# Kernel tuning notes

Hardware: AMD Instinct MI355X
Metric: run time of the kernel (lower is better)

The kernel has to match this reference:

```python
import math
import jax, jax.numpy as jnp
import numpy as np

B, H, W, CP = 64, 512, 512, 400
HALF_X = W // 2          # int, matches width//2 in the original
HALF_Y = H / 2.0         # float, matches height/2 in the original
NPTS = CP // 2
PI = math.pi


def fix_radians(tt):
    # Faithful translation of: -relu(-(2pi - relu(-tt)), threshold=-2pi) + relu(tt)
    inner = -(2.0 * PI - jnp.maximum(-tt, 0.0))
    thr = jnp.where(inner > -2.0 * PI, inner, 0.0)  # keras relu with threshold=-2pi
    return -thr + jnp.maximum(tt, 0.0)


def half_contour(pred_norm):
    # pred_norm: [B, H, W] in [0, 1]
    pred1st = jnp.round(pred_norm[:, :, :HALF_X])          # [B, H, W/2]
    x1st = jnp.sum(pred1st, axis=2)                        # [B, H] column count per row
    xaux = jnp.clip(x1st, 0.0, 1.0)                        # relu(.., threshold=0, max_value=1)
    ythtop = HALF_Y - jnp.sum(xaux[:, :HALF_X], axis=1)    # [B]
    ythbottom = HALF_Y + jnp.sum(xaux[:, HALF_X:], axis=1) # [B]
    rows = jnp.arange(W, dtype=pred_norm.dtype)[None, :]   # [1, W] (H == W assumed by original)
    # relu(rows - top) + top == max(rows, top); then min with bottom
    y1st = jnp.minimum(jnp.maximum(rows, ythtop[:, None]), ythbottom[:, None])  # [B, W]
    # Original: x1st <- half_x - x1st, then cart2pol(x1st - half_x, y1st - half_y)
    xc = -x1st                                             # [B, H]
    yc = y1st - HALF_Y                                     # [B, W]
    r1st = jnp.sqrt(xc ** 2 + yc ** 2)                     # [B, H]
    tt1st = fix_radians(jnp.arctan2(yc, xc))               # [B, H]

    tt_new = (PI / 2.0) + jnp.arange(NPTS, dtype=pred_norm.dtype) * (PI / NPTS)  # [NPTS]

    # RBF angular smoothing (get_rbf_points), with periodic wraparound copies
    tt_1 = jnp.concatenate([tt1st - 2.0 * PI, tt1st, tt1st + 2.0 * PI], axis=1)  # [B, 3H]
    r_cat = jnp.concatenate([r1st, r1st, r1st], axis=1)                          # [B, 3H]
    d2 = (tt_1[:, :, None] - tt_new[None, None, :]) ** 2                         # [B, 3H, NPTS]
    d2 = jnp.minimum(d2, 1.0)
    wgt = jnp.exp(-100.0 * d2)                                                   # [B, 3H, NPTS]
    wgt = wgt / jnp.sum(wgt, axis=1, keepdims=True)
    r_new = jnp.einsum('bkn,bk->bn', wgt, r_cat)                                 # [B, NPTS]

    x_new = r_new * jnp.cos(tt_new)[None, :] + HALF_X
    y_new = r_new * jnp.sin(tt_new)[None, :] + HALF_Y
    return jnp.stack([x_new, y_new], axis=-1)              # [B, NPTS, 2]


def setup_inputs() -> dict:
    key = jax.random.key(0)
    inputs = jax.random.uniform(key, (B, H, W, 2), dtype=jnp.float32)
    return {"inputs": inputs}


def reference(inputs) -> jnp.ndarray:
    lvc = inputs[:, :, :, -1]                              # [B, H, W]
    mn = jnp.min(lvc, axis=(1, 2), keepdims=True)
    mx = jnp.max(lvc, axis=(1, 2), keepdims=True)
    lvc_norm = (lvc - mn) / (mx - mn)
    c1 = half_contour(lvc_norm)                            # [B, NPTS, 2]
    c2 = half_contour(lvc_norm[:, :, ::-1])                # mirrored half
    c2 = jnp.concatenate([float(H) - c2[:, :, :1], c2[:, :, 1:]], axis=-1)[:, ::-1, :]
    return jnp.concatenate([c1, c2], axis=1)               # [B, CP, 2]
```

## Files before the change

kernel.cpp:

```cpp
#include <hip/hip_runtime.h>
#include <math.h>
#include <float.h>

#define BB 64
#define HH 512
#define WW 512
#define NPTS 200

#define PMIN_OFF 0
#define PMAX_OFF 2048
#define CNT_OFF  4224
#define TT_OFF   69760
#define RR_OFF   135296
#define SUMR_OFF 200832

__global__ __launch_bounds__(256) void kminmax(const float* __restrict__ in,
                                               float* __restrict__ ws) {
    int bid = blockIdx.x;
    int b   = bid >> 5;
    int c   = bid & 31;
    int t   = threadIdx.x;
    const float4* base = (const float4*)in + (size_t)b * 131072 + (size_t)c * 4096;
    float vmin = FLT_MAX, vmax = -FLT_MAX;
#pragma unroll
    for (int i = 0; i < 16; ++i) {
        float4 v = base[i * 256 + t];
        vmin = fminf(vmin, fminf(v.y, v.w));
        vmax = fmaxf(vmax, fmaxf(v.y, v.w));
    }
    for (int m = 32; m >= 1; m >>= 1) {
        vmin = fminf(vmin, __shfl_xor(vmin, m, 64));
        vmax = fmaxf(vmax, __shfl_xor(vmax, m, 64));
    }
    __shared__ float smin[4], smax[4];
    int wv = t >> 6;
    if ((t & 63) == 0) { smin[wv] = vmin; smax[wv] = vmax; }
    __syncthreads();
    if (t == 0) {
        float a = fminf(fminf(smin[0], smin[1]), fminf(smin[2], smin[3]));
        float z = fmaxf(fmaxf(smax[0], smax[1]), fmaxf(smax[2], smax[3]));
        ws[PMIN_OFF + bid] = a;
        ws[PMAX_OFF + bid] = z;
    }
}

__global__ __launch_bounds__(256) void kcount(const float* __restrict__ in,
                                              float* __restrict__ ws) {
    int gwave = (blockIdx.x * 256 + threadIdx.x) >> 6;
    int lane  = threadIdx.x & 63;
    int b     = gwave >> 9;
    int row   = gwave & 511;

    float mn = ws[PMIN_OFF + b * 32 + (lane & 31)];
    float mx = ws[PMAX_OFF + b * 32 + (lane & 31)];
    for (int m = 16; m >= 1; m >>= 1) {
        mn = fminf(mn, __shfl_xor(mn, m, 64));
        mx = fmaxf(mx, __shfl_xor(mx, m, 64));
    }
    float den = mx - mn;

    const float4* base = (const float4*)in + ((size_t)(b * HH + row)) * 256;
    int cl = 0, cr = 0;
#pragma unroll
    for (int i = 0; i < 4; ++i) {
        float4 v = base[i * 64 + lane];
        float t0 = (v.y - mn) / den;
        float t1 = (v.w - mn) / den;
        int c = (int)rintf(t0) + (int)rintf(t1);
        if (i < 2) cl += c; else cr += c;
    }
    for (int m = 32; m >= 1; m >>= 1) {
        cl += __shfl_xor(cl, m, 64);
        cr += __shfl_xor(cr, m, 64);
    }
    if (lane == 0) {
        ws[CNT_OFF + (b * 2 + 0) * 512 + row] = (float)cl;
        ws[CNT_OFF + (b * 2 + 1) * 512 + row] = (float)cr;
    }
}

__global__ __launch_bounds__(256) void kpolar(float* __restrict__ ws) {
    const float TWO_PI_F = 6.28318530717958647692f;
    const float PI_F     = 3.14159265358979323846f;
    int b2 = blockIdx.x;
    int t  = threadIdx.x;
    const float* cnt = ws + CNT_OFF + b2 * 512;
    float* tt_out    = ws + TT_OFF  + b2 * 512;
    float* rr_out    = ws + RR_OFF  + b2 * 512;

    __shared__ float s_red[12];

    float c0 = cnt[t];
    float c1 = cnt[t + 256];

    int r0 = (c0 >= 1.0f) ? 1 : 0;
    int r1 = (c1 >= 1.0f) ? 1 : 0;
    for (int m = 32; m >= 1; m >>= 1) {
        r0 += __shfl_xor(r0, m, 64);
        r1 += __shfl_xor(r1, m, 64);
    }
    int wv = t >> 6;
    if ((t & 63) == 0) { s_red[wv] = (float)r0; s_red[4 + wv] = (float)r1; }
    __syncthreads();
    float ythtop    = 256.0f - (s_red[0] + s_red[1] + s_red[2] + s_red[3]);
    float ythbottom = 256.0f + (s_red[4] + s_red[5] + s_red[6] + s_red[7]);

    float sumr_local = 0.0f;
#pragma unroll
    for (int j = 0; j < 2; ++j) {
        int   r  = t + j * 256;
        float x1 = (j == 0) ? c0 : c1;
        float y1 = fminf(fmaxf((float)r, ythtop), ythbottom);
        float xc = -x1;
        float yc = y1 - 256.0f;
        float rr = sqrtf(xc * xc + yc * yc);
        float tt;
        if (x1 == 0.0f && yc == 0.0f) {
            tt = PI_F;
        } else {
            tt = atan2f(yc, xc);
            if (tt < 0.0f) tt += TWO_PI_F;
        }
        tt_out[r] = tt;
        rr_out[r] = rr;
        sumr_local += rr;
    }
    float sr = sumr_local;
    for (int m = 32; m >= 1; m >>= 1) sr += __shfl_xor(sr, m, 64);
    if ((t & 63) == 0) s_red[8 + wv] = sr;
    __syncthreads();
    if (t == 0)
        ws[SUMR_OFF + b2] = s_red[8] + s_red[9] + s_red[10] + s_red[11];
}

__global__ __launch_bounds__(256) void kpoints(const float* __restrict__ ws,
                                               float* __restrict__ out) {
    int w    = (blockIdx.x * 256 + threadIdx.x) >> 6;
    int lane = threadIdx.x & 63;
    int b2   = w / NPTS;
    int t    = w - b2 * NPTS;
    int b    = b2 >> 1;
    int half = b2 & 1;

    const float4* ttv = (const float4*)(ws + TT_OFF + b2 * 512);
    const float4* rrv = (const float4*)(ws + RR_OFF + b2 * 512);
    float4 ta = ttv[lane], tb = ttv[lane + 64];
    float4 ra = rrv[lane], rb = rrv[lane + 64];
    float tts[8] = {ta.x, ta.y, ta.z, ta.w, tb.x, tb.y, tb.z, tb.w};
    float rs[8]  = {ra.x, ra.y, ra.z, ra.w, rb.x, rb.y, rb.z, rb.w};

    float ttn = 1.5707963267948966f + (float)t * 0.015707963267948966f;

    float d2[8];
    float dmin = 1.0f;
#pragma unroll
    for (int i = 0; i < 8; ++i) {
        float d = tts[i] - ttn;
        d2[i] = fminf(d * d, 1.0f);
        dmin = fminf(dmin, d2[i]);
    }
    for (int m = 32; m >= 1; m >>= 1) dmin = fminf(dmin, __shfl_xor(dmin, m, 64));

    float num = 0.0f, den = 0.0f;
#pragma unroll
    for (int i = 0; i < 8; ++i) {
        float wg = __expf(-100.0f * (d2[i] - dmin));
        den += wg;
        num += wg * rs[i];
    }
    for (int m = 32; m >= 1; m >>= 1) {
        den += __shfl_xor(den, m, 64);
        num += __shfl_xor(num, m, 64);
    }

    float sumr = ws[SUMR_OFF + b2];
    float w1 = __expf(-100.0f * (1.0f - dmin));
    den += 1024.0f * w1;
    num += 2.0f * w1 * sumr;

    float rn   = num / den;
    float xnew = rn * cosf(ttn) + 256.0f;
    float ynew = rn * sinf(ttn) + 256.0f;

    if (lane == 0) {
        if (half == 0) {
            out[((size_t)b * 400 + t) * 2 + 0] = xnew;
            out[((size_t)b * 400 + t) * 2 + 1] = ynew;
        } else {
            int p = 399 - t;
            out[((size_t)b * 400 + p) * 2 + 0] = 512.0f - xnew;
            out[((size_t)b * 400 + p) * 2 + 1] = ynew;
        }
    }
}

extern "C" void kernel_launch(void* const* d_in, const int* in_sizes, int n_in,
                              void* d_out, int out_size, void* d_ws, size_t ws_size,
                              hipStream_t stream) {
    const float* in  = (const float*)d_in[0];
    float*       out = (float*)d_out;
    float*       ws  = (float*)d_ws;

    kminmax<<<dim3(2048), dim3(256), 0, stream>>>(in, ws);
    kcount <<<dim3(8192), dim3(256), 0, stream>>>(in, ws);
    kpolar <<<dim3(128),  dim3(256), 0, stream>>>(ws);
    kpoints<<<dim3(6400), dim3(256), 0, stream>>>(ws, out);
}
```

Baseline: 222.3 us.

## Fuse polar conversion and RBF point evaluation into one kernel via shared memory

Merges the kpolar and kpoints kernels into a single kcontour kernel. Each block recomputes the polar angles and radii for its half-contour into shared memory, then loops over half of the output points with one wave per point. This drops one kernel launch and the global round trip for the theta/r arrays. In exchange the polar computation is done twice per half-contour, and only 256 blocks are launched instead of 6400, so less parallelism is exposed for the point evaluation.

```diff
diff --git a/kernel.cpp b/kernel.cpp
--- a/kernel.cpp
+++ b/kernel.cpp
@@ -10,9 +10,6 @@
 #define PMIN_OFF 0
 #define PMAX_OFF 2048
 #define CNT_OFF  4224
-#define TT_OFF   69760
-#define RR_OFF   135296
-#define SUMR_OFF 200832
 
 __global__ __launch_bounds__(256) void kminmax(const float* __restrict__ in,
                                                float* __restrict__ ws) {
@@ -79,117 +76,114 @@
     }
 }
 
-__global__ __launch_bounds__(256) void kpolar(float* __restrict__ ws) {
+__global__ __launch_bounds__(512) void kcontour(const float* __restrict__ ws,
+                                                float* __restrict__ out) {
     const float TWO_PI_F = 6.28318530717958647692f;
     const float PI_F     = 3.14159265358979323846f;
-    int b2 = blockIdx.x;
-    int t  = threadIdx.x;
+    int b2    = blockIdx.x >> 1;
+    int phase = blockIdx.x & 1;
+    int b     = b2 >> 1;
+    int half  = b2 & 1;
+    int tid   = threadIdx.x;
+    int wv    = tid >> 6;
+    int lane  = tid & 63;
+
     const float* cnt = ws + CNT_OFF + b2 * 512;
-    float* tt_out    = ws + TT_OFF  + b2 * 512;
-    float* rr_out    = ws + RR_OFF  + b2 * 512;
-
-    __shared__ float s_red[12];
-
-    float c0 = cnt[t];
-    float c1 = cnt[t + 256];
-
-    int r0 = (c0 >= 1.0f) ? 1 : 0;
-    int r1 = (c1 >= 1.0f) ? 1 : 0;
-    for (int m = 32; m >= 1; m >>= 1) {
-        r0 += __shfl_xor(r0, m, 64);
-        r1 += __shfl_xor(r1, m, 64);
-    }
-    int wv = t >> 6;
-    if ((t & 63) == 0) { s_red[wv] = (float)r0; s_red[4 + wv] = (float)r1; }
-    __syncthreads();
-    float ythtop    = 256.0f - (s_red[0] + s_red[1] + s_red[2] + s_red[3]);
-    float ythbottom = 256.0f + (s_red[4] + s_red[5] + s_red[6] + s_red[7]);
-
-    float sumr_local = 0.0f;
-#pragma unroll
-    for (int j = 0; j < 2; ++j) {
-        int   r  = t + j * 256;
-        float x1 = (j == 0) ? c0 : c1;
-        float y1 = fminf(fmaxf((float)r, ythtop), ythbottom);
-        float xc = -x1;
+
+    __shared__ __align__(16) float s_tt[512];
+    __shared__ __align__(16) float s_r[512];
+    __shared__ float s_red[8];
+    __shared__ float s_bc[3];
+
+    float c0 = cnt[tid];
+    int flag = (c0 >= 1.0f) ? 1 : 0;
+    int fs = flag;
+    for (int m = 32; m >= 1; m >>= 1) fs += __shfl_xor(fs, m, 64);
+    if (lane == 0) s_red[wv] = (float)fs;
+    __syncthreads();
+    if (tid == 0) {
+        s_bc[0] = 256.0f - (s_red[0] + s_red[1] + s_red[2] + s_red[3]);
+        s_bc[1] = 256.0f + (s_red[4] + s_red[5] + s_red[6] + s_red[7]);
+    }
+    __syncthreads();
+    float ythtop = s_bc[0], ythbottom = s_bc[1];
+
+    {
+        float y1 = fminf(fmaxf((float)tid, ythtop), ythbottom);
+        float xc = -c0;
         float yc = y1 - 256.0f;
         float rr = sqrtf(xc * xc + yc * yc);
         float tt;
-        if (x1 == 0.0f && yc == 0.0f) {
+        if (c0 == 0.0f && yc == 0.0f) {
             tt = PI_F;
         } else {
             tt = atan2f(yc, xc);
             if (tt < 0.0f) tt += TWO_PI_F;
         }
-        tt_out[r] = tt;
-        rr_out[r] = rr;
-        sumr_local += rr;
-    }
-    float sr = sumr_local;
-    for (int m = 32; m >= 1; m >>= 1) sr += __shfl_xor(sr, m, 64);
-    if ((t & 63) == 0) s_red[8 + wv] = sr;
-    __syncthreads();
-    if (t == 0)
-        ws[SUMR_OFF + b2] = s_red[8] + s_red[9] + s_red[10] + s_red[11];
-}
-
-__global__ __launch_bounds__(256) void kpoints(const float* __restrict__ ws,
-                                               float* __restrict__ out) {
-    int w    = (blockIdx.x * 256 + threadIdx.x) >> 6;
-    int lane = threadIdx.x & 63;
-    int b2   = w / NPTS;
-    int t    = w - b2 * NPTS;
-    int b    = b2 >> 1;
-    int half = b2 & 1;
-
-    const float4* ttv = (const float4*)(ws + TT_OFF + b2 * 512);
-    const float4* rrv = (const float4*)(ws + RR_OFF + b2 * 512);
+        s_tt[tid] = tt;
+        s_r[tid]  = rr;
+        float sr = rr;
+        for (int m = 32; m >= 1; m >>= 1) sr += __shfl_xor(sr, m, 64);
+        if (lane == 0) s_red[wv] = sr;
+    }
+    __syncthreads();
+    if (tid == 0)
+        s_bc[2] = s_red[0] + s_red[1] + s_red[2] + s_red[3] +
+                  s_red[4] + s_red[5] + s_red[6] + s_red[7];
+    __syncthreads();
+    float sumr = s_bc[2];
+
+    const float4* ttv = (const float4*)s_tt;
+    const float4* rrv = (const float4*)s_r;
     float4 ta = ttv[lane], tb = ttv[lane + 64];
     float4 ra = rrv[lane], rb = rrv[lane + 64];
     float tts[8] = {ta.x, ta.y, ta.z, ta.w, tb.x, tb.y, tb.z, tb.w};
     float rs[8]  = {ra.x, ra.y, ra.z, ra.w, rb.x, rb.y, rb.z, rb.w};
 
-    float ttn = 1.5707963267948966f + (float)t * 0.015707963267948966f;
-
-    float d2[8];
-    float dmin = 1.0f;
-#pragma unroll
-    for (int i = 0; i < 8; ++i) {
-        float d = tts[i] - ttn;
-        d2[i] = fminf(d * d, 1.0f);
-        dmin = fminf(dmin, d2[i]);
-    }
-    for (int m = 32; m >= 1; m >>= 1) dmin = fminf(dmin, __shfl_xor(dmin, m, 64));
-
-    float num = 0.0f, den = 0.0f;
-#pragma unroll
-    for (int i = 0; i < 8; ++i) {
-        float wg = __expf(-100.0f * (d2[i] - dmin));
-        den += wg;
-        num += wg * rs[i];
-    }
-    for (int m = 32; m >= 1; m >>= 1) {
-        den += __shfl_xor(den, m, 64);
-        num += __shfl_xor(num, m, 64);
-    }
-
-    float sumr = ws[SUMR_OFF + b2];
-    float w1 = __expf(-100.0f * (1.0f - dmin));
-    den += 1024.0f * w1;
-    num += 2.0f * w1 * sumr;
-
-    float rn   = num / den;
-    float xnew = rn * cosf(ttn) + 256.0f;
-    float ynew = rn * sinf(ttn) + 256.0f;
-
-    if (lane == 0) {
-        if (half == 0) {
-            out[((size_t)b * 400 + t) * 2 + 0] = xnew;
-            out[((size_t)b * 400 + t) * 2 + 1] = ynew;
-        } else {
-            int p = 399 - t;
-            out[((size_t)b * 400 + p) * 2 + 0] = 512.0f - xnew;
-            out[((size_t)b * 400 + p) * 2 + 1] = ynew;
+    int pbase = phase * 100;
+    for (int p = pbase + wv; p < pbase + 100; p += 8) {
+        float ttn = 1.5707963267948966f + (float)p * 0.015707963267948966f;
+
+        float d2[8];
+        float dmin = 1.0f;
+#pragma unroll
+        for (int i = 0; i < 8; ++i) {
+            float d = tts[i] - ttn;
+            d2[i] = fminf(d * d, 1.0f);
+            dmin = fminf(dmin, d2[i]);
+        }
+        for (int m = 32; m >= 1; m >>= 1)
+            dmin = fminf(dmin, __shfl_xor(dmin, m, 64));
+
+        float num = 0.0f, den = 0.0f;
+#pragma unroll
+        for (int i = 0; i < 8; ++i) {
+            float wg = __expf(-100.0f * (d2[i] - dmin));
+            den += wg;
+            num += wg * rs[i];
+        }
+        for (int m = 32; m >= 1; m >>= 1) {
+            den += __shfl_xor(den, m, 64);
+            num += __shfl_xor(num, m, 64);
+        }
+
+        float w1 = __expf(-100.0f * (1.0f - dmin));
+        den += 1024.0f * w1;
+        num += 2.0f * w1 * sumr;
+
+        float rn   = num / den;
+        float xnew = rn * cosf(ttn) + 256.0f;
+        float ynew = rn * sinf(ttn) + 256.0f;
+
+        if (lane == 0) {
+            if (half == 0) {
+                out[((size_t)b * 400 + p) * 2 + 0] = xnew;
+                out[((size_t)b * 400 + p) * 2 + 1] = ynew;
+            } else {
+                int q = 399 - p;
+                out[((size_t)b * 400 + q) * 2 + 0] = 512.0f - xnew;
+                out[((size_t)b * 400 + q) * 2 + 1] = ynew;
+            }
         }
     }
 }
@@ -201,8 +195,7 @@
     float*       out = (float*)d_out;
     float*       ws  = (float*)d_ws;
 
-    kminmax<<<dim3(2048), dim3(256), 0, stream>>>(in, ws);
-    kcount <<<dim3(8192), dim3(256), 0, stream>>>(in, ws);
-    kpolar <<<dim3(128),  dim3(256), 0, stream>>>(ws);
-    kpoints<<<dim3(6400), dim3(256), 0, stream>>>(ws, out);
-}
+    kminmax <<<dim3(2048), dim3(256), 0, stream>>>(in, ws);
+    kcount  <<<dim3(8192), dim3(256), 0, stream>>>(in, ws);
+    kcontour<<<dim3(256),  dim3(512), 0, stream>>>(ws, out);
+}
```

After: 221.0 us. Within noise of the previous version (-0.6%).
